# Performance work log

Hardware: AMD Instinct MI355X
Metric: run time of the kernel (lower is better)

Reference implementation:

```python
import jax, jax.numpy as jnp
import numpy as np
from jax import lax

N_NODES = 100000
N_EDGES = 3200000
NODE_DIM = 128
K = 8            # number of kmeans heads
MAX_OVERLAP = 2  # top-k cluster memberships per node
THRESH = 1e-8


def setup_inputs() -> dict:
    key = jax.random.key(0)
    k1, k2, k3, k4, k5 = jax.random.split(key, 5)
    x = jax.random.normal(k1, (N_NODES, NODE_DIM), dtype=jnp.float32)
    edge_index = jax.random.randint(k2, (2, N_EDGES), 0, N_NODES, dtype=jnp.int64)
    # binary initial cluster-membership masks [N, K] (float, like KMeansCarry.mask)
    mask = (jax.random.uniform(k3, (N_NODES, K)) > 0.5).astype(jnp.float32)
    Ww = jax.random.normal(k4, (K, NODE_DIM, NODE_DIM), dtype=jnp.float32) * (1.0 / np.sqrt(NODE_DIM))
    Wm = jax.random.normal(k5, (K, NODE_DIM, 1), dtype=jnp.float32) * (1.0 / np.sqrt(NODE_DIM))
    return {"x": x, "edge_index": edge_index, "mask": mask, "Ww": Ww, "Wm": Wm}


def reference(x, edge_index, mask, Ww, Wm):
    """KMeans over graph: k heads -> boolean node scores -> norm-weighted top-k assignment."""
    N = x.shape[0]
    src, dst = edge_index[0], edge_index[1]

    def head(m_col, Ww_i, Wm_i):
        # masked node features (KMeansCarry.masked_x)
        xm = x * m_col[:, None]                                   # [N, D]
        node_mask = m_col > 0                                     # [N]
        # masked subgraph (KMeansCarry.masked_edge_index): keep edges with both endpoints in mask
        ev = (node_mask[src] & node_mask[dst]).astype(x.dtype)    # [E]
        # weighting module: per-node transform
        w = jax.nn.relu(xm @ Ww_i)                                # [N, D]
        # message passing over masked subgraph (irregular gather/scatter)
        agg = jax.ops.segment_sum(w[src] * ev[:, None], dst, num_segments=N)  # [N, D]
        # mask module score -> act -> threshold at 0 (KMeansHead.forward)
        score = ((xm + agg) @ Wm_i)[:, 0]                         # [N]
        return jnp.tanh(score) > 0                                # bool [N]

    # vmap over the K heads
    head_masks = jax.vmap(head, in_axes=(1, 0, 0), out_axes=1)(mask, Ww, Wm)  # [N, K] bool

    # KMeans.forward combine step
    above_thresh = head_masks  # bool > THRESH (1e-8 < 1) == the bool itself
    norms = jnp.linalg.norm(x, axis=1, keepdims=True)             # [N, 1]
    masked_weights = jnp.where(above_thresh, norms, -jnp.inf)     # [N, K]
    top_vals, top_idx = lax.top_k(masked_weights, MAX_OVERLAP)    # [N, MAX_OVERLAP]
    valid = jnp.isfinite(top_vals)
    # scatter ones at (row, top_idx) where valid  (duplicate-safe via one-hot + min)
    oh = jax.nn.one_hot(top_idx, K, dtype=x.dtype) * valid[..., None].astype(x.dtype)
    final_mask = jnp.minimum(oh.sum(axis=1), 1.0)                 # [N, K]
    return final_mask
```

## Files before the change

kernel.cpp:

```cpp
#include <hip/hip_runtime.h>

#define N_NODES 100000
#define N_EDGES 3200000
#define D 128
#define K 8

#define TAU 4e-3f
#define WL_CAP 262144

#define CHUNK 96
#define GWAVES 8

#define BKT 128
#define NB  ((N_NODES + BKT - 1) / BKT)
#define EPB 16384
#define NEB ((N_EDGES + EPB - 1) / EPB)

typedef float  f32x4  __attribute__((ext_vector_type(4)));
typedef __bf16 bf16x8 __attribute__((ext_vector_type(8)));

static __device__ __forceinline__ unsigned short bfbits(float f)
{
    const __bf16 b = (__bf16)f;
    return __builtin_bit_cast(unsigned short, b);
}
static __device__ __forceinline__ float bfback(unsigned short u)
{
    return (float)__builtin_bit_cast(__bf16, u);
}

__global__ __launch_bounds__(256)
void compact_kernel(const float* __restrict__ mask,
                    int* __restrict__ lists,
                    int* __restrict__ cnts,
                    unsigned char* __restrict__ mb)
{
    __shared__ int wcnt[4][K];
    __shared__ int wbase[4][K];

    const int n = blockIdx.x * 256 + threadIdx.x;
    const int lane = threadIdx.x & 63;
    const int wave = threadIdx.x >> 6;
    const bool valid = (n < N_NODES);

    unsigned long long ball[K];
    int bits8 = 0;
    #pragma unroll
    for (int k = 0; k < K; ++k) {
        const bool m = valid && (mask[(size_t)n * K + k] > 0.0f);
        bits8 |= m ? (1 << k) : 0;
        ball[k] = __ballot(m);
        if (lane == 0) wcnt[wave][k] = __popcll(ball[k]);
    }
    __syncthreads();

    if (threadIdx.x < K) {
        const int k = threadIdx.x;
        const int t0 = wcnt[0][k], t1 = wcnt[1][k], t2 = wcnt[2][k], t3 = wcnt[3][k];
        const int base = (t0 + t1 + t2 + t3)
                       ? atomicAdd(&cnts[k], t0 + t1 + t2 + t3) : 0;
        wbase[0][k] = base;
        wbase[1][k] = base + t0;
        wbase[2][k] = base + t0 + t1;
        wbase[3][k] = base + t0 + t1 + t2;
    }
    __syncthreads();

    #pragma unroll
    for (int k = 0; k < K; ++k) {
        if ((ball[k] >> lane) & 1ull) {
            const int pos = __popcll(ball[k] & ((1ull << lane) - 1ull));
            lists[(size_t)k * N_NODES + wbase[wave][k] + pos] = n;
        }
    }
    if (valid) mb[n] = (unsigned char)bits8;
}

__global__ __launch_bounds__(256)
void wsplit_kernel(const float* __restrict__ Ww,
                   unsigned short* __restrict__ wtH,
                   unsigned short* __restrict__ wtL)
{
    const int t = blockIdx.x * 256 + threadIdx.x;
    if (t >= K * D * D) return;
    const int k   = t >> 14;
    const int kk  = (t >> 7) & 127;
    const int col = t & 127;
    const float v = Ww[t];
    const __bf16 h = (__bf16)v;
    const __bf16 l = (__bf16)(v - (float)h);
    const int o = (k << 14) | (col << 7) | kk;
    wtH[o] = __builtin_bit_cast(unsigned short, h);
    wtL[o] = __builtin_bit_cast(unsigned short, l);
}

__global__ __launch_bounds__(512, 4)
void head_gemm_kernel(const float* __restrict__ x,
                      const unsigned short* __restrict__ wtH,
                      const unsigned short* __restrict__ wtL,
                      const float* __restrict__ Wm,
                      const int* __restrict__ lists,
                      const int* __restrict__ cnts,
                      float* __restrict__ t32,
                      float* __restrict__ base32)
{
    __shared__ __align__(16) unsigned short Ah[CHUNK * D];
    __shared__ __align__(16) unsigned short Al[CHUNK * D];
    __shared__ float redT[GWAVES][48];
    __shared__ float redB[CHUNK][4];
    __shared__ int   ids[CHUNK];

    const int bid = blockIdx.x;
    const int k = (bid >> 3) & 7;
    const int c = ((bid >> 6) << 3) | (bid & 7);

    const int cnt = cnts[k];
    const int nbase = c * CHUNK;
    if (nbase >= cnt) return;

    const int tid = threadIdx.x;
    const int lane = tid & 63;
    const int wave = __builtin_amdgcn_readfirstlane((int)(tid >> 6));
    const int* list = lists + (size_t)k * N_NODES;

    if (tid < CHUNK) {
        int idx = nbase + tid;
        if (idx >= cnt) idx = cnt - 1;
        ids[tid] = list[idx];
    }
    __syncthreads();

    if (tid < CHUNK * 4) {
        const int r = tid >> 2;
        const int q = tid & 3;
        const int id = ids[r];
        const float4* xr  = (const float4*)(x + (size_t)id * D);
        const float4* wm4 = (const float4*)(Wm + k * D);
        float bp = 0.0f;
        #pragma unroll
        for (int i = 0; i < 8; ++i) {
            const int f4 = q + 4 * i;
            const float4 v  = xr[f4];
            const float4 wv = wm4[f4];
            bp += v.x * wv.x + v.y * wv.y + v.z * wv.z + v.w * wv.w;
            ushort4 h, l;
            h.x = bfbits(v.x); l.x = bfbits(v.x - bfback(h.x));
            h.y = bfbits(v.y); l.y = bfbits(v.y - bfback(h.y));
            h.z = bfbits(v.z); l.z = bfbits(v.z - bfback(h.z));
            h.w = bfbits(v.w); l.w = bfbits(v.w - bfback(h.w));
            const int boff = ((r * 256 + f4 * 8) ^ ((r & 7) << 4)) >> 1;
            *(ushort4*)&Ah[boff] = h;
            *(ushort4*)&Al[boff] = l;
        }
        redB[r][q] = bp;
    }
    __syncthreads();

    const int wm_ = wave >> 2;
    const int wn  = wave & 3;
    const int l15 = lane & 15;
    const int lg  = lane >> 4;
    const int n0  = wn * 32;

    f32x4 acc[3][2];
    #pragma unroll
    for (int mf = 0; mf < 3; ++mf) {
        acc[mf][0] = (f32x4){0.f, 0.f, 0.f, 0.f};
        acc[mf][1] = (f32x4){0.f, 0.f, 0.f, 0.f};
    }

    const unsigned short* bH0 = wtH + (((k * D + n0 + l15) << 7) + 8 * lg);
    const unsigned short* bH1 = bH0 + (16 << 7);
    const unsigned short* bL0 = wtL + (((k * D + n0 + l15) << 7) + 8 * lg);
    const unsigned short* bL1 = bL0 + (16 << 7);

    #pragma unroll
    for (int s = 0; s < 4; ++s) {
        const int ko = s * 32;
        const bf16x8 Bh0 = *reinterpret_cast<const bf16x8*>(bH0 + ko);
        const bf16x8 Bh1 = *reinterpret_cast<const bf16x8*>(bH1 + ko);
        const bf16x8 Bl0 = *reinterpret_cast<const bf16x8*>(bL0 + ko);
        const bf16x8 Bl1 = *reinterpret_cast<const bf16x8*>(bL1 + ko);
        #pragma unroll
        for (int mf = 0; mf < 3; ++mf) {
            const int m = wm_ * 48 + mf * 16 + l15;
            const int byt = (m * 256 + (ko + 8 * lg) * 2) ^ ((m & 7) << 4);
            const bf16x8 Amh = *reinterpret_cast<const bf16x8*>(&Ah[byt >> 1]);
            const bf16x8 Aml = *reinterpret_cast<const bf16x8*>(&Al[byt >> 1]);
            acc[mf][0] = __builtin_amdgcn_mfma_f32_16x16x32_bf16(Amh, Bh0, acc[mf][0], 0, 0, 0);
            acc[mf][1] = __builtin_amdgcn_mfma_f32_16x16x32_bf16(Amh, Bh1, acc[mf][1], 0, 0, 0);
            acc[mf][0] = __builtin_amdgcn_mfma_f32_16x16x32_bf16(Amh, Bl0, acc[mf][0], 0, 0, 0);
            acc[mf][1] = __builtin_amdgcn_mfma_f32_16x16x32_bf16(Amh, Bl1, acc[mf][1], 0, 0, 0);
            acc[mf][0] = __builtin_amdgcn_mfma_f32_16x16x32_bf16(Aml, Bh0, acc[mf][0], 0, 0, 0);
            acc[mf][1] = __builtin_amdgcn_mfma_f32_16x16x32_bf16(Aml, Bh1, acc[mf][1], 0, 0, 0);
        }
    }

    const float wmv0 = Wm[k * D + n0 + l15];
    const float wmv1 = Wm[k * D + n0 + 16 + l15];
    float keep = 0.0f;
    #pragma unroll
    for (int mf = 0; mf < 3; ++mf) {
        #pragma unroll
        for (int r = 0; r < 4; ++r) {
            float p = fmaxf(acc[mf][0][r], 0.0f) * wmv0
                    + fmaxf(acc[mf][1][r], 0.0f) * wmv1;
            p += __shfl_xor(p, 1);
            p += __shfl_xor(p, 2);
            p += __shfl_xor(p, 4);
            p += __shfl_xor(p, 8);
            if (l15 == mf * 4 + r) keep = p;
        }
    }
    if (l15 < 12)
        redT[wave][((l15 >> 2) << 4) + (lg << 2) + (l15 & 3)] = keep;
    __syncthreads();

    if (tid < CHUNK) {
        const int r = tid;
        const int idx = nbase + r;
        if (idx < cnt) {
            const int wg = r / 48;
            const int rl = r - wg * 48;
            const float ts = redT[wg * 4 + 0][rl] + redT[wg * 4 + 1][rl]
                           + redT[wg * 4 + 2][rl] + redT[wg * 4 + 3][rl];
            const float bs = redB[r][0] + redB[r][1] + redB[r][2] + redB[r][3];
            const int id = ids[r];
            t32[(size_t)id * K + k]    = ts;
            base32[(size_t)id * K + k] = bs;
        }
    }
}

__global__ __launch_bounds__(256)
void ehist_kernel(const int* __restrict__ ei, int* __restrict__ bhist)
{
    __shared__ int lh[NB];
    const int tid = threadIdx.x;
    for (int i = tid; i < NB; i += 256) lh[i] = 0;
    __syncthreads();
    const int e0 = blockIdx.x * EPB;
    #pragma unroll 4
    for (int i = 0; i < EPB / 256; ++i) {
        const int e = e0 + i * 256 + tid;
        if (e < N_EDGES) {
            const int d = ei[(long long)N_EDGES + e];
            atomicAdd(&lh[d >> 7], 1);
        }
    }
    __syncthreads();
    for (int i = tid; i < NB; i += 256) {
        const int c = lh[i];
        if (c) atomicAdd(&bhist[i], c);
    }
}

__global__ __launch_bounds__(1024)
void escan_kernel(const int* __restrict__ bhist,
                  int* __restrict__ bases,
                  int* __restrict__ cursors)
{
    __shared__ int sc[1024];
    const int tid = threadIdx.x;
    const int v = (tid < NB) ? bhist[tid] : 0;
    sc[tid] = v;
    __syncthreads();
    for (int off = 1; off < 1024; off <<= 1) {
        int t = 0;
        if (tid >= off) t = sc[tid - off];
        __syncthreads();
        sc[tid] += t;
        __syncthreads();
    }
    if (tid < NB) {
        const int ex = sc[tid] - v;
        bases[tid]   = ex;
        cursors[tid] = ex;
        if (tid == NB - 1) bases[NB] = sc[tid];
    }
}

__global__ __launch_bounds__(512)
void ebucket_kernel(const int* __restrict__ ei,
                    int* __restrict__ cursors,
                    int* __restrict__ bkt)
{
    __shared__ int lh[NB];
    __shared__ int wb[NB];
    const int tid = threadIdx.x;
    for (int i = tid; i < NB; i += 512) lh[i] = 0;
    __syncthreads();
    const int e0 = blockIdx.x * EPB;
    #pragma unroll 4
    for (int i = 0; i < EPB / 512; ++i) {
        const int e = e0 + i * 512 + tid;
        if (e < N_EDGES) atomicAdd(&lh[ei[(long long)N_EDGES + e] >> 7], 1);
    }
    __syncthreads();
    for (int i = tid; i < NB; i += 512) {
        const int c = lh[i];
        wb[i] = c ? atomicAdd(&cursors[i], c) : 0;
        lh[i] = 0;
    }
    __syncthreads();
    #pragma unroll 4
    for (int i = 0; i < EPB / 512; ++i) {
        const int e = e0 + i * 512 + tid;
        if (e < N_EDGES) {
            const int d = ei[(long long)N_EDGES + e];
            const int s = ei[e];
            const int b = d >> 7;
            const int r = atomicAdd(&lh[b], 1);
            const int idx = wb[b] + r;
            if (idx < N_EDGES)
                bkt[idx] = (s << 7) | (d & 127);
        }
    }
}

__global__ __launch_bounds__(512)
void eaccum_kernel(const int* __restrict__ bkt,
                   const int* __restrict__ bases,
                   const unsigned char* __restrict__ mb,
                   const float* __restrict__ t32,
                   const float* __restrict__ base32,
                   float* __restrict__ agg32,
                   float* __restrict__ out,
                   unsigned char* __restrict__ flag8,
                   double* __restrict__ s64,
                   int2* __restrict__ wl,
                   int* __restrict__ wlcnt)
{
    __shared__ float acc[BKT * K];
    __shared__ unsigned char mbl[BKT];
    __shared__ unsigned char fll[BKT];
    __shared__ int anyfl;
    const int b = blockIdx.x;
    const int n0 = b << 7;
    const int tid = threadIdx.x;
    for (int i = tid; i < BKT * K; i += 512) acc[i] = 0.0f;
    if (tid < BKT) {
        const int n = n0 + tid;
        mbl[tid] = (n < N_NODES) ? mb[n] : 0;
    }
    if (tid == 0) anyfl = 0;
    __syncthreads();

    const int eB = bases[b];
    int eE = bases[b + 1];
    if (eE > N_EDGES) eE = N_EDGES;
    for (int e = eB + tid; e < eE; e += 512) {
        const int rec = bkt[e];
        const int s  = rec >> 7;
        const int dl = rec & 127;
        const unsigned md = mbl[dl];
        if (md) {
            const float4* tr = (const float4*)(t32 + (size_t)s * K);
            const float4 t0 = tr[0], t1 = tr[1];
            #pragma unroll
            for (int k = 0; k < K; ++k) {
                const float tv = (k < 4)
                    ? ((k < 2) ? (k == 0 ? t0.x : t0.y) : (k == 2 ? t0.z : t0.w))
                    : ((k < 6) ? (k == 4 ? t1.x : t1.y) : (k == 6 ? t1.z : t1.w));
                if (((md >> k) & 1) && tv != 0.0f)
                    atomicAdd(&acc[(dl << 3) + k], tv);
            }
        }
    }
    __syncthreads();

    if (tid < BKT) {
        const int n = n0 + tid;
        if (n < N_NODES) {
            const unsigned m8 = mbl[tid];
            const float4* b4 = (const float4*)(base32 + (size_t)n * K);
            const float4 b40 = b4[0], b41 = b4[1];
            float bs[K];
            bs[0] = b40.x; bs[1] = b40.y; bs[2] = b40.z; bs[3] = b40.w;
            bs[4] = b41.x; bs[5] = b41.y; bs[6] = b41.z; bs[7] = b41.w;
            float o[K];
            int cnt = 0, fl = 0;
            #pragma unroll
            for (int k = 0; k < K; ++k) {
                const float sc = bs[k] + acc[(tid << 3) + k];
                const bool masked = (m8 >> k) & 1;
                const bool hm = masked && (sc > 0.0f);
                if (masked && fabsf(sc) < TAU) fl |= (1 << k);
                o[k] = (hm && cnt < 2) ? 1.0f : 0.0f;
                cnt += hm ? 1 : 0;
            }
            float4* op = (float4*)(out + (size_t)n * K);
            op[0] = make_float4(o[0], o[1], o[2], o[3]);
            op[1] = make_float4(o[4], o[5], o[6], o[7]);
            float4* ap = (float4*)(agg32 + (size_t)n * K);
            ap[0] = make_float4(acc[(tid << 3) + 0], acc[(tid << 3) + 1],
                                acc[(tid << 3) + 2], acc[(tid << 3) + 3]);
            ap[1] = make_float4(acc[(tid << 3) + 4], acc[(tid << 3) + 5],
                                acc[(tid << 3) + 6], acc[(tid << 3) + 7]);
            flag8[n] = (unsigned char)fl;
            fll[tid] = (unsigned char)fl;
            if (fl) {
                anyfl = 1;
                #pragma unroll
                for (int k = 0; k < K; ++k)
                    if ((fl >> k) & 1) s64[(size_t)n * K + k] = 0.0;
            }
        } else {
            fll[tid] = 0;
        }
    }
    __syncthreads();

    if (anyfl) {
        for (int e = eB + tid; e < eE; e += 512) {
            const int rec = bkt[e];
            const int dl = rec & 127;
            unsigned f = fll[dl];
            if (!f) continue;
            const int s = rec >> 7;
            f &= mb[s];
            while (f) {
                const int k = __ffs(f) - 1;
                f &= f - 1;
                const int idx = atomicAdd(wlcnt, 1);
                if (idx < WL_CAP) wl[idx] = make_int2(s | (k << 20), n0 + dl);
            }
        }
    }
}

__global__ __launch_bounds__(256)
void scatter_fallback_kernel(const int* __restrict__ ei,
                             const unsigned char* __restrict__ mb,
                             const float* __restrict__ t32,
                             float* __restrict__ agg32)
{
    const long long tid = (long long)blockIdx.x * 256 + threadIdx.x;
    if (tid >= (long long)N_EDGES * K) return;
    const int k = (int)(tid & (K - 1));
    const long long e = tid >> 3;
    const int d = ei[(long long)N_EDGES + e];
    const int s = ei[e];
    const unsigned md = mb[d] & mb[s];
    if (!((md >> k) & 1)) return;
    const float v = t32[(size_t)s * K + k];
    if (v != 0.0f) atomicAdd(&agg32[(size_t)d * K + k], v);
}

__global__ __launch_bounds__(256)
void combine_flag_kernel(const unsigned char* __restrict__ mb,
                         const float* __restrict__ base32,
                         const float* __restrict__ agg32,
                         float* __restrict__ out,
                         unsigned char* __restrict__ flag8,
                         double* __restrict__ s64)
{
    const int n = blockIdx.x * 256 + threadIdx.x;
    if (n >= N_NODES) return;
    const unsigned m8 = mb[n];
    float o[K];
    int cnt = 0, fl = 0;
    #pragma unroll
    for (int k = 0; k < K; ++k) {
        const float s = base32[(size_t)n * K + k] + agg32[(size_t)n * K + k];
        const bool masked = (m8 >> k) & 1;
        const bool hm = masked && (s > 0.0f);
        if (masked && fabsf(s) < TAU) fl |= (1 << k);
        o[k] = (hm && cnt < 2) ? 1.0f : 0.0f;
        cnt += hm ? 1 : 0;
    }
    float4* op = (float4*)(out + (size_t)n * K);
    op[0] = make_float4(o[0], o[1], o[2], o[3]);
    op[1] = make_float4(o[4], o[5], o[6], o[7]);
    flag8[n] = (unsigned char)fl;
    if (fl) {
        #pragma unroll
        for (int k = 0; k < K; ++k)
            if ((fl >> k) & 1) s64[(size_t)n * K + k] = 0.0;
    }
}

__global__ __launch_bounds__(256)
void edge_flag_kernel(const int* __restrict__ ei,
                      const unsigned char* __restrict__ mb,
                      const unsigned char* __restrict__ flag8,
                      int2* __restrict__ wl,
                      int* __restrict__ wlcnt)
{
    const int e = blockIdx.x * 256 + threadIdx.x;
    if (e >= N_EDGES) return;
    const int d = ei[(long long)N_EDGES + e];
    unsigned f = flag8[d];
    if (!f) return;
    const int s = ei[e];
    f &= mb[s];
    while (f) {
        const int k = __ffs(f) - 1;
        f &= f - 1;
        const int idx = atomicAdd(wlcnt, 1);
        if (idx < WL_CAP) wl[idx] = make_int2(s | (k << 20), d);
    }
}

__global__ __launch_bounds__(256)
void repair_t_kernel(const float* __restrict__ x,
                     const float* __restrict__ Ww,
                     const float* __restrict__ Wm,
                     const int2* __restrict__ wl,
                     const int* __restrict__ wlcnt,
                     double* __restrict__ score64)
{
    const int lane = threadIdx.x & 63;
    const int waveId = blockIdx.x * 4 + (threadIdx.x >> 6);
    const int nWaves = gridDim.x * 4;
    int cnt = *wlcnt;
    if (cnt > WL_CAP) cnt = WL_CAP;
    for (int w = waveId; w < cnt; w += nWaves) {
        const int2 ent = wl[w];
        const int s = __builtin_amdgcn_readfirstlane(ent.x & 0xFFFFF);
        const int k = __builtin_amdgcn_readfirstlane(ent.x >> 20);
        const int d = ent.y;
        const float* xr = x + (size_t)s * D;
        const float* Wk = Ww + (size_t)k * D * D;
        double c0 = 0.0, c1 = 0.0;
        for (int j = 0; j < D; ++j) {
            const double xd = (double)xr[j];
            c0 = fma(xd, (double)Wk[j * D + lane], c0);
            c1 = fma(xd, (double)Wk[j * D + lane + 64], c1);
        }
        double ts = fmax(c0, 0.0) * (double)Wm[k * D + lane]
                  + fmax(c1, 0.0) * (double)Wm[k * D + lane + 64];
        #pragma unroll
        for (int off = 32; off > 0; off >>= 1) ts += __shfl_xor(ts, off);
        if (lane == 0) atomicAdd(&score64[(size_t)d * K + k], ts);
    }
}

__global__ __launch_bounds__(256)
void repair_combine_kernel(const float* __restrict__ x,
                           const unsigned char* __restrict__ mb,
                           const float* __restrict__ Wm,
                           const float* __restrict__ base32,
                           const float* __restrict__ agg32,
                           const double* __restrict__ score64,
                           const unsigned char* __restrict__ flag8,
                           float* __restrict__ out)
{
    const int n = blockIdx.x * 256 + threadIdx.x;
    if (n >= N_NODES) return;
    const unsigned f = flag8[n];
    if (!f) return;
    const unsigned m8 = mb[n];
    float o[K];
    int cnt = 0;
    #pragma unroll
    for (int k = 0; k < K; ++k) {
        bool hm;
        if ((f >> k) & 1) {
            double b = 0.0;
            for (int j = 0; j < D; ++j)
                b = fma((double)x[(size_t)n * D + j], (double)Wm[k * D + j], b);
            hm = (b + score64[(size_t)n * K + k]) > 0.0;
        } else {
            hm = ((m8 >> k) & 1) &&
                 ((base32[(size_t)n * K + k] + agg32[(size_t)n * K + k]) > 0.0f);
        }
        o[k] = (hm && cnt < 2) ? 1.0f : 0.0f;
        cnt += hm ? 1 : 0;
    }
    float4* op = (float4*)(out + (size_t)n * K);
    op[0] = make_float4(o[0], o[1], o[2], o[3]);
    op[1] = make_float4(o[4], o[5], o[6], o[7]);
}

extern "C" void kernel_launch(void* const* d_in, const int* in_sizes, int n_in,
                              void* d_out, int out_size, void* d_ws, size_t ws_size,
                              hipStream_t stream)
{
    const float* x    = (const float*)d_in[0];
    const int*   ei   = (const int*)d_in[1];
    const float* mask = (const float*)d_in[2];
    const float* Ww   = (const float*)d_in[3];
    const float* Wm   = (const float*)d_in[4];
    float* out = (float*)d_out;

    char* w = (char*)d_ws;
    float*          t32    = (float*)w;
    float*          agg32  = (float*)(w + 3200000);
    double*         s64    = (double*)(w + 6400000);
    int*            lists  = (int*)(w + 6400000);
    unsigned short* wtH    = (unsigned short*)(w + 9600000);
    unsigned short* wtL    = (unsigned short*)(w + 9600000 + 262144);
    unsigned char*  flag8  = (unsigned char*)(w + 12800000);
    int*            cnts   = (int*)(w + 12900000);
    int*            wlcnt  = (int*)(w + 12900032);
    int*            bhist  = (int*)(w + 12900064);
    int*            bases  = (int*)(w + 12903200);
    int*            cursors= (int*)(w + 12906336);
    int2*           wl     = (int2*)(w + 12909504);
    float*          b32    = (float*)(w + 15006656);
    unsigned char*  mb     = (unsigned char*)(w + 18206656);
    int*            bkt    = (int*)(w + 18306656);
    const size_t WS_BUCKETED = 31106656;
    const bool bucketed = (ws_size >= WS_BUCKETED);

    hipMemsetAsync(t32, 0, 3200000, stream);
    hipMemsetAsync(w + 12900000, 0, 4096, stream);

    wsplit_kernel<<<(K * D * D + 255) / 256, 256, 0, stream>>>(Ww, wtH, wtL);

    compact_kernel<<<(N_NODES + 255) / 256, 256, 0, stream>>>(mask, lists, cnts, mb);

    const int nchunks = (N_NODES + CHUNK - 1) / CHUNK;
    const int nc8 = (nchunks + 7) & ~7;
    head_gemm_kernel<<<nc8 * K, 512, 0, stream>>>(x, wtH, wtL, Wm, lists, cnts, t32, b32);

    if (bucketed) {
        ehist_kernel<<<NEB, 256, 0, stream>>>(ei, bhist);
        escan_kernel<<<1, 1024, 0, stream>>>(bhist, bases, cursors);
        ebucket_kernel<<<NEB, 512, 0, stream>>>(ei, cursors, bkt);
        eaccum_kernel<<<NB, 512, 0, stream>>>(bkt, bases, mb, t32, b32,
                                              agg32, out, flag8, s64, wl, wlcnt);
    } else {
        hipMemsetAsync(agg32, 0, 3200000, stream);
        const long long nek = (long long)N_EDGES * K;
        scatter_fallback_kernel<<<(int)((nek + 255) / 256), 256, 0, stream>>>(
            ei, mb, t32, agg32);
        combine_flag_kernel<<<(N_NODES + 255) / 256, 256, 0, stream>>>(
            mb, b32, agg32, out, flag8, s64);
        edge_flag_kernel<<<(N_EDGES + 255) / 256, 256, 0, stream>>>(
            ei, mb, flag8, wl, wlcnt);
    }

    repair_t_kernel<<<512, 256, 0, stream>>>(x, Ww, Wm, wl, wlcnt, s64);

    repair_combine_kernel<<<(N_NODES + 255) / 256, 256, 0, stream>>>(
        x, mb, Wm, b32, agg32, s64, flag8, out);
}
```

Before: 379.3 us.

## Pre-split x into bf16 hi/lo once and stream into LDS via global_load_lds

```diff
diff --git a/kernel.cpp b/kernel.cpp
--- a/kernel.cpp
+++ b/kernel.cpp
@@ -13,7 +13,7 @@
 
 #define BKT 128
 #define NB  ((N_NODES + BKT - 1) / BKT)
-#define EPB 16384
+#define EPB 8192
 #define NEB ((N_EDGES + EPB - 1) / EPB)
 
 typedef float  f32x4  __attribute__((ext_vector_type(4)));
@@ -27,6 +27,13 @@
 static __device__ __forceinline__ float bfback(unsigned short u)
 {
     return (float)__builtin_bit_cast(__bf16, u);
+}
+
+static __device__ __forceinline__ void gload_lds16(const void* g, void* l)
+{
+    __builtin_amdgcn_global_load_lds(
+        (const __attribute__((address_space(1))) unsigned int*)g,
+        (__attribute__((address_space(3))) unsigned int*)l, 16, 0, 0);
 }
 
 __global__ __launch_bounds__(256)
@@ -94,15 +101,193 @@
     wtL[o] = __builtin_bit_cast(unsigned short, l);
 }
 
+__global__ __launch_bounds__(256)
+void xsplit_kernel(const float* __restrict__ x,
+                   const float* __restrict__ Wm,
+                   unsigned short* __restrict__ xh,
+                   unsigned short* __restrict__ xl,
+                   float* __restrict__ b32)
+{
+    __shared__ float wm[K * D];
+    __shared__ float red[64][4][K];
+    const int tid = threadIdx.x;
+    const int n0 = blockIdx.x * 64;
+    for (int i = tid; i < K * D; i += 256) wm[i] = Wm[i];
+    __syncthreads();
+
+    const int row = tid >> 2;
+    const int q   = tid & 3;
+    const int n   = n0 + row;
+    float bp[K];
+    #pragma unroll
+    for (int k = 0; k < K; ++k) bp[k] = 0.0f;
+
+    if (n < N_NODES) {
+        const float4* xr = (const float4*)(x + (size_t)n * D);
+        #pragma unroll
+        for (int i = 0; i < 8; ++i) {
+            const int f4 = q + 4 * i;
+            const float4 v = xr[f4];
+            ushort4 h, l;
+            h.x = bfbits(v.x); l.x = bfbits(v.x - bfback(h.x));
+            h.y = bfbits(v.y); l.y = bfbits(v.y - bfback(h.y));
+            h.z = bfbits(v.z); l.z = bfbits(v.z - bfback(h.z));
+            h.w = bfbits(v.w); l.w = bfbits(v.w - bfback(h.w));
+            *(ushort4*)(xh + (size_t)n * D + f4 * 4) = h;
+            *(ushort4*)(xl + (size_t)n * D + f4 * 4) = l;
+            const int j0 = f4 * 4;
+            #pragma unroll
+            for (int k = 0; k < K; ++k)
+                bp[k] += v.x * wm[k * D + j0]     + v.y * wm[k * D + j0 + 1]
+                       + v.z * wm[k * D + j0 + 2] + v.w * wm[k * D + j0 + 3];
+        }
+    }
+    #pragma unroll
+    for (int k = 0; k < K; ++k) red[row][q][k] = bp[k];
+    __syncthreads();
+
+    for (int t = tid; t < 64 * K; t += 256) {
+        const int rr = t >> 3;
+        const int k  = t & 7;
+        const int nn = n0 + rr;
+        if (nn < N_NODES)
+            b32[(size_t)nn * K + k] = red[rr][0][k] + red[rr][1][k]
+                                    + red[rr][2][k] + red[rr][3][k];
+    }
+}
+
 __global__ __launch_bounds__(512, 4)
-void head_gemm_kernel(const float* __restrict__ x,
+void head_gemm_kernel(const unsigned short* __restrict__ xh,
+                      const unsigned short* __restrict__ xl,
                       const unsigned short* __restrict__ wtH,
                       const unsigned short* __restrict__ wtL,
                       const float* __restrict__ Wm,
                       const int* __restrict__ lists,
                       const int* __restrict__ cnts,
-                      float* __restrict__ t32,
-                      float* __restrict__ base32)
+                      float* __restrict__ t32)
+{
+    __shared__ __align__(16) unsigned short Ah[CHUNK * D];
+    __shared__ __align__(16) unsigned short Al[CHUNK * D];
+    __shared__ float redT[GWAVES][48];
+    __shared__ int   ids[CHUNK];
+
+    const int bid = blockIdx.x;
+    const int k = (bid >> 3) & 7;
+    const int c = ((bid >> 6) << 3) | (bid & 7);
+
+    const int cnt = cnts[k];
+    const int nbase = c * CHUNK;
+    if (nbase >= cnt) return;
+
+    const int tid = threadIdx.x;
+    const int lane = tid & 63;
+    const int wave = __builtin_amdgcn_readfirstlane((int)(tid >> 6));
+    const int* list = lists + (size_t)k * N_NODES;
+
+    if (tid < CHUNK) {
+        int idx = nbase + tid;
+        if (idx >= cnt) idx = cnt - 1;
+        ids[tid] = list[idx];
+    }
+    __syncthreads();
+
+    {
+        #pragma unroll
+        for (int j = 0; j < 3; ++j) {
+            const int R = wave * 12 + j * 4;
+            const int r = R + (lane >> 4);
+            const int id = ids[r];
+            const int so = (((lane & 15) ^ (r & 7)) << 4);
+            gload_lds16((const char*)(xh + (size_t)id * D) + so,
+                        (char*)Ah + R * 256);
+            gload_lds16((const char*)(xl + (size_t)id * D) + so,
+                        (char*)Al + R * 256);
+        }
+    }
+    __syncthreads();
+
+    const int wm_ = wave >> 2;
+    const int wn  = wave & 3;
+    const int l15 = lane & 15;
+    const int lg  = lane >> 4;
+    const int n0  = wn * 32;
+
+    f32x4 acc[3][2];
+    #pragma unroll
+    for (int mf = 0; mf < 3; ++mf) {
+        acc[mf][0] = (f32x4){0.f, 0.f, 0.f, 0.f};
+        acc[mf][1] = (f32x4){0.f, 0.f, 0.f, 0.f};
+    }
+
+    const unsigned short* bH0 = wtH + (((k * D + n0 + l15) << 7) + 8 * lg);
+    const unsigned short* bH1 = bH0 + (16 << 7);
+    const unsigned short* bL0 = wtL + (((k * D + n0 + l15) << 7) + 8 * lg);
+    const unsigned short* bL1 = bL0 + (16 << 7);
+
+    #pragma unroll
+    for (int s = 0; s < 4; ++s) {
+        const int ko = s * 32;
+        const bf16x8 Bh0 = *reinterpret_cast<const bf16x8*>(bH0 + ko);
+        const bf16x8 Bh1 = *reinterpret_cast<const bf16x8*>(bH1 + ko);
+        const bf16x8 Bl0 = *reinterpret_cast<const bf16x8*>(bL0 + ko);
+        const bf16x8 Bl1 = *reinterpret_cast<const bf16x8*>(bL1 + ko);
+        #pragma unroll
+        for (int mf = 0; mf < 3; ++mf) {
+            const int m = wm_ * 48 + mf * 16 + l15;
+            const int byt = (m * 256 + (ko + 8 * lg) * 2) ^ ((m & 7) << 4);
+            const bf16x8 Amh = *reinterpret_cast<const bf16x8*>(&Ah[byt >> 1]);
+            const bf16x8 Aml = *reinterpret_cast<const bf16x8*>(&Al[byt >> 1]);
+            acc[mf][0] = __builtin_amdgcn_mfma_f32_16x16x32_bf16(Amh, Bh0, acc[mf][0], 0, 0, 0);
+            acc[mf][1] = __builtin_amdgcn_mfma_f32_16x16x32_bf16(Amh, Bh1, acc[mf][1], 0, 0, 0);
+            acc[mf][0] = __builtin_amdgcn_mfma_f32_16x16x32_bf16(Amh, Bl0, acc[mf][0], 0, 0, 0);
+            acc[mf][1] = __builtin_amdgcn_mfma_f32_16x16x32_bf16(Amh, Bl1, acc[mf][1], 0, 0, 0);
+            acc[mf][0] = __builtin_amdgcn_mfma_f32_16x16x32_bf16(Aml, Bh0, acc[mf][0], 0, 0, 0);
+            acc[mf][1] = __builtin_amdgcn_mfma_f32_16x16x32_bf16(Aml, Bh1, acc[mf][1], 0, 0, 0);
+        }
+    }
+
+    const float wmv0 = Wm[k * D + n0 + l15];
+    const float wmv1 = Wm[k * D + n0 + 16 + l15];
+    float keep = 0.0f;
+    #pragma unroll
+    for (int mf = 0; mf < 3; ++mf) {
+        #pragma unroll
+        for (int r = 0; r < 4; ++r) {
+            float p = fmaxf(acc[mf][0][r], 0.0f) * wmv0
+                    + fmaxf(acc[mf][1][r], 0.0f) * wmv1;
+            p += __shfl_xor(p, 1);
+            p += __shfl_xor(p, 2);
+            p += __shfl_xor(p, 4);
+            p += __shfl_xor(p, 8);
+            if (l15 == mf * 4 + r) keep = p;
+        }
+    }
+    if (l15 < 12)
+        redT[wave][((l15 >> 2) << 4) + (lg << 2) + (l15 & 3)] = keep;
+    __syncthreads();
+
+    if (tid < CHUNK) {
+        const int r = tid;
+        const int idx = nbase + r;
+        if (idx < cnt) {
+            const int wg = r / 48;
+            const int rl = r - wg * 48;
+            const float ts = redT[wg * 4 + 0][rl] + redT[wg * 4 + 1][rl]
+                           + redT[wg * 4 + 2][rl] + redT[wg * 4 + 3][rl];
+            t32[(size_t)ids[r] * K + k] = ts;
+        }
+    }
+}
+
+__global__ __launch_bounds__(512, 4)
+void head_gemm_f32_kernel(const float* __restrict__ x,
+                          const unsigned short* __restrict__ wtH,
+                          const unsigned short* __restrict__ wtL,
+                          const float* __restrict__ Wm,
+                          const int* __restrict__ lists,
+                          const int* __restrict__ cnts,
+                          float* __restrict__ t32,
+                          float* __restrict__ base32)
 {
     __shared__ __align__(16) unsigned short Ah[CHUNK * D];
     __shared__ __align__(16) unsigned short Al[CHUNK * D];
@@ -232,24 +417,24 @@
     }
 }
 
-__global__ __launch_bounds__(256)
+__global__ __launch_bounds__(512)
 void ehist_kernel(const int* __restrict__ ei, int* __restrict__ bhist)
 {
     __shared__ int lh[NB];
     const int tid = threadIdx.x;
-    for (int i = tid; i < NB; i += 256) lh[i] = 0;
+    for (int i = tid; i < NB; i += 512) lh[i] = 0;
     __syncthreads();
     const int e0 = blockIdx.x * EPB;
     #pragma unroll 4
-    for (int i = 0; i < EPB / 256; ++i) {
-        const int e = e0 + i * 256 + tid;
+    for (int i = 0; i < EPB / 512; ++i) {
+        const int e = e0 + i * 512 + tid;
         if (e < N_EDGES) {
             const int d = ei[(long long)N_EDGES + e];
             atomicAdd(&lh[d >> 7], 1);
         }
     }
     __syncthreads();
-    for (int i = tid; i < NB; i += 256) {
+    for (int i = tid; i < NB; i += 512) {
         const int c = lh[i];
         if (c) atomicAdd(&bhist[i], c);
     }
@@ -601,8 +786,12 @@
     float*          b32    = (float*)(w + 15006656);
     unsigned char*  mb     = (unsigned char*)(w + 18206656);
     int*            bkt    = (int*)(w + 18306656);
+    unsigned short* xh     = (unsigned short*)(w + 31106688);
+    unsigned short* xl     = (unsigned short*)(w + 56706688);
     const size_t WS_BUCKETED = 31106656;
+    const size_t WS_XSPLIT   = 82306688;
     const bool bucketed = (ws_size >= WS_BUCKETED);
+    const bool xsplit   = (ws_size >= WS_XSPLIT);
 
     hipMemsetAsync(t32, 0, 3200000, stream);
     hipMemsetAsync(w + 12900000, 0, 4096, stream);
@@ -613,10 +802,17 @@
 
     const int nchunks = (N_NODES + CHUNK - 1) / CHUNK;
     const int nc8 = (nchunks + 7) & ~7;
-    head_gemm_kernel<<<nc8 * K, 512, 0, stream>>>(x, wtH, wtL, Wm, lists, cnts, t32, b32);
+    if (xsplit) {
+        xsplit_kernel<<<(N_NODES + 63) / 64, 256, 0, stream>>>(x, Wm, xh, xl, b32);
+        head_gemm_kernel<<<nc8 * K, 512, 0, stream>>>(xh, xl, wtH, wtL, Wm,
+                                                      lists, cnts, t32);
+    } else {
+        head_gemm_f32_kernel<<<nc8 * K, 512, 0, stream>>>(x, wtH, wtL, Wm,
+                                                          lists, cnts, t32, b32);
+    }
 
     if (bucketed) {
-        ehist_kernel<<<NEB, 256, 0, stream>>>(ei, bhist);
+        ehist_kernel<<<NEB, 512, 0, stream>>>(ei, bhist);
         escan_kernel<<<1, 1024, 0, stream>>>(bhist, bases, cursors);
         ebucket_kernel<<<NEB, 512, 0, stream>>>(ei, cursors, bkt);
         eaccum_kernel<<<NB, 512, 0, stream>>>(bkt, bases, mb, t32, b32,
```

New measurement: 396.1 us. 4.5% more time.
